# Kernel optimization log

Measured on AMD Instinct MI355X. Metric: run time of the kernel, lower is better.

Reference implementation:

```python
import jax, jax.numpy as jnp
import numpy as np
from jax import lax

BS, T, NN, F_IN = 4, 32, 128, 64
HID, HEADS, NC, LD, RH = 64, 4, 32, 64, 256
E = 2048
NEG_SLOPE = 0.2


def setup_inputs() -> dict:
    key = jax.random.key(0)
    ks = jax.random.split(key, 20)
    f32 = jnp.float32
    def n(k, shape, s=0.05):
        return jax.random.normal(k, shape, f32) * s
    G4 = 4 * RH
    return {
        "x": jax.random.normal(ks[0], (BS, T, NN, F_IN), f32),
        "edge_index": jax.random.randint(ks[1], (2, E), 0, NN),
        "W1": n(ks[2], (F_IN, HEADS * HID)),
        "as1": n(ks[3], (HEADS, HID)), "ad1": n(ks[4], (HEADS, HID)),
        "b1": jnp.zeros((HEADS * HID,), f32),
        "W2": n(ks[5], (HEADS * HID, HEADS * HID)),
        "as2": n(ks[6], (HEADS, HID)), "ad2": n(ks[7], (HEADS, HID)),
        "b2": jnp.zeros((HEADS * HID,), f32),
        "W3": n(ks[8], (HEADS * HID, HID)),
        "as3": n(ks[9], (1, HID)), "ad3": n(ks[10], (1, HID)),
        "b3": jnp.zeros((HID,), f32),
        "Wih_f": n(ks[11], (G4, HID)), "Whh_f": n(ks[12], (G4, RH)),
        "bih_f": jnp.zeros((G4,), f32), "bhh_f": jnp.zeros((G4,), f32),
        "Wih_b": n(ks[13], (G4, HID)), "Whh_b": n(ks[14], (G4, RH)),
        "bih_b": jnp.zeros((G4,), f32), "bhh_b": jnp.zeros((G4,), f32),
        "Wmu": n(ks[15], (NC * LD, 2 * RH)), "bmu": jnp.zeros((NC * LD,), f32),
        "Wlv": n(ks[16], (NC * LD, 2 * RH)), "blv": jnp.zeros((NC * LD,), f32),
        "Wpi": n(ks[17], (NC, 2 * RH)), "bpi": jnp.zeros((NC,), f32),
    }


def _lstm_dir(seq, Wih, Whh, bih, bhh, rh):
    # seq: [T, B, D]; torch gate order i, f, g, o
    B = seq.shape[1]
    h0 = jnp.zeros((B, rh), seq.dtype)
    c0 = jnp.zeros((B, rh), seq.dtype)
    def step(carry, xt):
        h, c = carry
        g = xt @ Wih.T + h @ Whh.T + bih + bhh
        i, f, gg, o = jnp.split(g, 4, axis=-1)
        c = jax.nn.sigmoid(f) * c + jax.nn.sigmoid(i) * jnp.tanh(gg)
        h = jax.nn.sigmoid(o) * jnp.tanh(c)
        return (h, c), None
    (hT, _), _ = lax.scan(step, (h0, c0), seq)
    return hT


def reference(x, edge_index, W1, as1, ad1, b1, W2, as2, ad2, b2,
              W3, as3, ad3, b3,
              Wih_f, Whh_f, bih_f, bhh_f, Wih_b, Whh_b, bih_b, bhh_b,
              Wmu, bmu, Wlv, blv, Wpi, bpi):
    bs, T_, nn_, fin = x.shape
    G = bs * T_
    N = G * nn_
    xt = x.reshape(N, fin)
    # batch the per-graph edge list with node offsets, then add self loops (PyG default)
    off = jnp.arange(G, dtype=edge_index.dtype) * nn_
    src = (edge_index[0][None, :] + off[:, None]).reshape(-1)
    dst = (edge_index[1][None, :] + off[:, None]).reshape(-1)
    loop = jnp.arange(N, dtype=edge_index.dtype)
    src = jnp.concatenate([src, loop])
    dst = jnp.concatenate([dst, loop])

    def gat(h_in, W, a_s, a_d, b, heads):
        C = W.shape[1] // heads
        h = (h_in @ W).reshape(N, heads, C)
        a_src = jnp.sum(h * a_s, axis=-1)  # [N, H]
        a_dst = jnp.sum(h * a_d, axis=-1)
        e = jax.nn.leaky_relu(a_src[src] + a_dst[dst], NEG_SLOPE)  # [Etot, H]
        m = jax.ops.segment_max(e, dst, num_segments=N)
        m = jnp.where(jnp.isfinite(m), m, 0.0)
        ex = jnp.exp(e - m[dst])
        den = jax.ops.segment_sum(ex, dst, num_segments=N)
        alpha = ex / (den[dst] + 1e-16)
        out = jax.ops.segment_sum(alpha[:, :, None] * h[src], dst, num_segments=N)
        return out.reshape(N, heads * C) + b

    h = jax.nn.relu(gat(xt, W1, as1, ad1, b1, HEADS))
    h = jax.nn.relu(gat(h, W2, as2, ad2, b2, HEADS))
    h = jax.nn.relu(gat(h, W3, as3, ad3, b3, 1))

    batch_idx = jnp.repeat(jnp.arange(G), nn_)
    graph_embs = jax.ops.segment_sum(h, batch_idx, num_segments=G).reshape(bs, T_, -1)
    seq = jnp.transpose(graph_embs, (1, 0, 2))  # [T, B, D]
    h_f = _lstm_dir(seq, Wih_f, Whh_f, bih_f, bhh_f, RH)
    h_b = _lstm_dir(seq[::-1], Wih_b, Whh_b, bih_b, bhh_b, RH)
    feat = jnp.concatenate([h_f, h_b], axis=-1)  # [B, 2*RH]
    mu = (feat @ Wmu.T + bmu).reshape(bs, NC, LD)
    logvar = (feat @ Wlv.T + blv).reshape(bs, NC, LD)
    pi_logits = feat @ Wpi.T + bpi
    return (mu, logvar, pi_logits)
```

## Files before the change

### kernel.cpp

```cpp
#include <hip/hip_runtime.h>
#include <hip/hip_bf16.h>
#include <cstdint>

#define NLOC 128
#define NGRAPH 128
#define NNODE 16384
#define EBASE 2048

typedef _Float16 half2v __attribute__((ext_vector_type(2)));
typedef _Float16 f16x8 __attribute__((ext_vector_type(8)));
typedef float f32x4 __attribute__((ext_vector_type(4)));

__device__ __forceinline__ float sigf(float x) { return 1.f / (1.f + __expf(-x)); }
__device__ __forceinline__ float tanhfast(float x) {
    float e = __expf(2.f * x);
    return 1.f - 2.f / (e + 1.f);
}
__device__ __forceinline__ uint32_t packh2(float a, float b) {
    half2v v;
    v.x = (_Float16)a; v.y = (_Float16)b;
    return __builtin_bit_cast(uint32_t, v);
}
__device__ __forceinline__ float dot2(uint32_t w, uint32_t h, float acc) {
#if __has_builtin(__builtin_amdgcn_fdot2)
    return __builtin_amdgcn_fdot2(__builtin_bit_cast(half2v, w),
                                  __builtin_bit_cast(half2v, h), acc, false);
#else
    half2v wv = __builtin_bit_cast(half2v, w);
    half2v hv = __builtin_bit_cast(half2v, h);
    return acc + (float)wv.x * (float)hv.x + (float)wv.y * (float)hv.y;
#endif
}

__global__ __launch_bounds__(256) void prep_kernel(const int* __restrict__ ei,
                                                   float* __restrict__ Adj,
                                                   const float* __restrict__ Whh_f,
                                                   const float* __restrict__ Whh_b,
                                                   uint32_t* __restrict__ wreg,
                                                   uint32_t* __restrict__ wtail) {
    int b = blockIdx.x, tid = threadIdx.x;
    if (b < 128) {
        __shared__ int rowA[NLOC];
        int v = b;
        if (tid < NLOC) rowA[tid] = 0;
        __syncthreads();
        const int* srcs = ei;
        const int* dsts = ei + EBASE;
        int e0 = tid * 8;
#pragma unroll
        for (int k = 0; k < 8; ++k)
            if (dsts[e0 + k] == v) atomicAdd(&rowA[srcs[e0 + k]], 1);
        __syncthreads();
        if (tid < NLOC) Adj[v * NLOC + tid] = (float)rowA[tid] + (tid == v ? 1.f : 0.f);
    } else {
        int gid = (b - 128) * 256 + tid;
        int dir = gid >> 10, row = gid & 1023;
        const float* src = (dir ? Whh_b : Whh_f) + (size_t)row * 256;
        uint4* wr4 = (uint4*)wreg;
#pragma unroll
        for (int i = 0; i < 24; ++i) {
            uint4 v;
            v.x = packh2(src[i * 8 + 0], src[i * 8 + 1]);
            v.y = packh2(src[i * 8 + 2], src[i * 8 + 3]);
            v.z = packh2(src[i * 8 + 4], src[i * 8 + 5]);
            v.w = packh2(src[i * 8 + 6], src[i * 8 + 7]);
            wr4[(size_t)(dir * 24 + i) * 1024 + row] = v;
        }
        uint4* wt4 = (uint4*)wtail;
#pragma unroll
        for (int ku = 0; ku < 8; ++ku) {
            const float* s8 = src + 192 + ku * 8;
            uint4 v;
            v.x = packh2(s8[0], s8[1]);
            v.y = packh2(s8[2], s8[3]);
            v.z = packh2(s8[4], s8[5]);
            v.w = packh2(s8[6], s8[7]);
            wt4[(size_t)(dir * 8 + ku) * 1024 + row] = v;
        }
    }
}

template <int K, int NL, int NF, bool POOLX>
__global__ __launch_bounds__(512) void fl_kernel(const float* __restrict__ A,
                                                 const float* __restrict__ Wg,
                                                 const float* __restrict__ a_s,
                                                 const float* __restrict__ a_d,
                                                 const float* __restrict__ Adj,
                                                 const float* __restrict__ bias,
                                                 const float* __restrict__ Wih_f, const float* __restrict__ bif, const float* __restrict__ bhf,
                                                 const float* __restrict__ Wih_b, const float* __restrict__ bib, const float* __restrict__ bhb,
                                                 float* __restrict__ outG) {
    constexpr int HL = NL / 64;
    constexpr int NT = NL / 64;
    constexpr int WPH = 4 / HL;
    constexpr int NLSH = (NL == 128) ? 7 : 6;
    constexpr int LDA = K + 4;
    constexpr int LDB = 68;
    constexpr int LDH = 136;
    constexpr int ASB = 128 * LDA * 2;
    constexpr int HTB = NL * LDH * 2;
    constexpr int R1 = (ASB > HTB) ? ASB : HTB;
    constexpr int R2 = 128 * LDH * 2;
    __shared__ __align__(16) char raw[R1 + R2];
    _Float16* As = (_Float16*)raw;
    _Float16* Ht = (_Float16*)raw;
    _Float16* Bs = (_Float16*)(raw + R1);
    _Float16* Wt = (_Float16*)(raw + R1);
    __shared__ float as_l[128 * HL];
    __shared__ float ad_l[128 * HL];
    __shared__ float den_l[128];
    __shared__ float as_part[4][128];
    __shared__ float ad_part[4][128];
    __shared__ float psum[8][64];
    __shared__ float emb[64];

    int g = blockIdx.x, tid = threadIdx.x;
    int foff = blockIdx.y * NL;
    int lane = tid & 63, w = tid >> 6;
    int wm = w >> 2, wn = w & 3;
    int col = lane & 15, kg = lane >> 4;
    size_t base = (size_t)g * 128;

    float asc[NT], adc[NT];
#pragma unroll
    for (int nt = 0; nt < NT; ++nt) {
        int f = foff + (wn * NT + nt) * 16 + col;
        asc[nt] = a_s[f];
        adc[nt] = a_d[f];
    }
    {
        const float* src = A + base * K;
        for (int i = tid; i < 128 * K / 2; i += 512) {
            int m = (2 * i) / K, k = (2 * i) % K;
            float2 v = *(const float2*)(src + (size_t)m * K + k);
            *(uint32_t*)&As[m * LDA + k] = packh2(v.x, v.y);
        }
    }
    f32x4 acc[4][NT];
#pragma unroll
    for (int mt = 0; mt < 4; ++mt)
#pragma unroll
        for (int nt = 0; nt < NT; ++nt) acc[mt][nt] = (f32x4){0.f, 0.f, 0.f, 0.f};
#pragma unroll 1
    for (int kc = 0; kc < K / 64; ++kc) {
        __syncthreads();
        for (int j = tid; j < NL * 32; j += 512) {
            int n = j & (NL - 1), kk = j >> NLSH;
            int k = kc * 64 + 2 * kk;
            float w0 = Wg[(size_t)k * NF + foff + n];
            float w1 = Wg[(size_t)(k + 1) * NF + foff + n];
            *(uint32_t*)&Bs[n * LDB + 2 * kk] = packh2(w0, w1);
        }
        __syncthreads();
        uint4 bf[NT][2];
#pragma unroll
        for (int nt = 0; nt < NT; ++nt) {
            int nb = (wn * NT + nt) * 16 + col;
            bf[nt][0] = *(const uint4*)&Bs[nb * LDB + kg * 8];
            bf[nt][1] = *(const uint4*)&Bs[nb * LDB + 32 + kg * 8];
        }
#pragma unroll
        for (int mt = 0; mt < 4; ++mt) {
            int mrow = wm * 64 + mt * 16 + col;
            uint4 a0 = *(const uint4*)&As[mrow * LDA + kc * 64 + kg * 8];
            uint4 a1 = *(const uint4*)&As[mrow * LDA + kc * 64 + 32 + kg * 8];
#pragma unroll
            for (int nt = 0; nt < NT; ++nt) {
                acc[mt][nt] = __builtin_amdgcn_mfma_f32_16x16x32_f16(
                    __builtin_bit_cast(f16x8, a0), __builtin_bit_cast(f16x8, bf[nt][0]),
                    acc[mt][nt], 0, 0, 0);
                acc[mt][nt] = __builtin_amdgcn_mfma_f32_16x16x32_f16(
                    __builtin_bit_cast(f16x8, a1), __builtin_bit_cast(f16x8, bf[nt][1]),
                    acc[mt][nt], 0, 0, 0);
            }
        }
    }
    __syncthreads();
#pragma unroll
    for (int mt = 0; mt < 4; ++mt) {
        int mb = wm * 64 + mt * 16;
        float pas[4] = {0.f, 0.f, 0.f, 0.f}, pdd[4] = {0.f, 0.f, 0.f, 0.f};
#pragma unroll
        for (int nt = 0; nt < NT; ++nt) {
#pragma unroll
            for (int r = 0; r < 4; ++r) {
                float hv = acc[mt][nt][r];
                pas[r] += hv * asc[nt];
                pdd[r] += hv * adc[nt];
            }
            int f = (wn * NT + nt) * 16 + col;
            *(uint32_t*)&Ht[f * LDH + mb + kg * 4] = packh2(acc[mt][nt][0], acc[mt][nt][1]);
            *(uint32_t*)&Ht[f * LDH + mb + kg * 4 + 2] = packh2(acc[mt][nt][2], acc[mt][nt][3]);
        }
#pragma unroll
        for (int off = 1; off < 16; off <<= 1)
#pragma unroll
            for (int r = 0; r < 4; ++r) {
                pas[r] += __shfl_xor(pas[r], off, 64);
                pdd[r] += __shfl_xor(pdd[r], off, 64);
            }
        if (col == 0) {
#pragma unroll
            for (int r = 0; r < 4; ++r) {
                int m = mb + kg * 4 + r;
                as_part[wn][m] = pas[r];
                ad_part[wn][m] = pdd[r];
            }
        }
    }
    __syncthreads();
    if (tid < 128) {
#pragma unroll
        for (int hl = 0; hl < HL; ++hl) {
            float sa = 0.f, sd = 0.f;
#pragma unroll
            for (int q = 0; q < WPH; ++q) {
                sa += as_part[hl * WPH + q][tid];
                sd += ad_part[hl * WPH + q][tid];
            }
            as_l[tid * HL + hl] = sa;
            ad_l[tid * HL + hl] = sd;
        }
    }
    __syncthreads();
    for (int h = 0; h < HL; ++h) {
        {
            int v = tid >> 2, ub = (tid & 3) * 32;
            float advv = ad_l[v * HL + h];
            const float* arow = Adj + (size_t)v * 128 + ub;
            float dsum = 0.f;
#pragma unroll
            for (int j = 0; j < 16; ++j) {
                float a0 = arow[2 * j], a1 = arow[2 * j + 1];
                float e0 = as_l[(ub + 2 * j) * HL + h] + advv;
                float e1 = as_l[(ub + 2 * j + 1) * HL + h] + advv;
                e0 = (e0 > 0.f) ? e0 : 0.2f * e0;
                e1 = (e1 > 0.f) ? e1 : 0.2f * e1;
                float w0 = a0 * __expf(e0);
                float w1 = a1 * __expf(e1);
                dsum += w0 + w1;
                *(uint32_t*)&Wt[v * LDH + ub + 2 * j] = packh2(w0, w1);
            }
            dsum += __shfl_xor(dsum, 1, 64);
            dsum += __shfl_xor(dsum, 2, 64);
            if ((tid & 3) == 0) den_l[v] = dsum;
        }
        __syncthreads();
        {
            int vt = w;
            f16x8 af[4];
#pragma unroll
            for (int kt = 0; kt < 4; ++kt) {
                uint4 au = *(const uint4*)&Wt[(vt * 16 + col) * LDH + kt * 32 + kg * 8];
                af[kt] = __builtin_bit_cast(f16x8, au);
            }
            float dn[4];
#pragma unroll
            for (int r = 0; r < 4; ++r) dn[r] = den_l[vt * 16 + kg * 4 + r] + 1e-16f;
#pragma unroll
            for (int ft = 0; ft < 4; ++ft) {
                int f = h * 64 + ft * 16 + col;
                f32x4 oacc = {0.f, 0.f, 0.f, 0.f};
#pragma unroll
                for (int kt = 0; kt < 4; ++kt) {
                    uint4 bu = *(const uint4*)&Ht[f * LDH + kt * 32 + kg * 8];
                    oacc = __builtin_amdgcn_mfma_f32_16x16x32_f16(
                        af[kt], __builtin_bit_cast(f16x8, bu), oacc, 0, 0, 0);
                }
                float bv = bias[foff + f];
                if constexpr (!POOLX) {
#pragma unroll
                    for (int r = 0; r < 4; ++r) {
                        int v = vt * 16 + kg * 4 + r;
                        float o = oacc[r] / dn[r] + bv;
                        outG[(size_t)(base + v) * NF + foff + f] = fmaxf(o, 0.f);
                    }
                } else {
                    float ps = 0.f;
#pragma unroll
                    for (int r = 0; r < 4; ++r) ps += fmaxf(oacc[r] / dn[r] + bv, 0.f);
                    ps += __shfl_xor(ps, 16, 64);
                    ps += __shfl_xor(ps, 32, 64);
                    if (kg == 0) psum[w][f] = ps;
                }
            }
        }
        __syncthreads();
    }
    if constexpr (POOLX) {
        if (tid < 64) {
            float s = 0.f;
#pragma unroll
            for (int q = 0; q < 8; ++q) s += psum[q][tid];
            emb[tid] = s;
        }
        __syncthreads();
        int rrow = (g & 31) * 4 + (g >> 5);
        for (int dir = 0; dir < 2; ++dir) {
            const float* W = dir ? Wih_b : Wih_f;
            const float* bi = dir ? bib : bif;
            const float* bh = dir ? bhb : bhf;
            for (int o = tid; o < 1024; o += 512) {
                const float* wr = W + (size_t)o * 64;
                float s = bi[o] + bh[o];
#pragma unroll
                for (int k = 0; k < 64; k += 4) {
                    float4 wv = *(const float4*)(wr + k);
                    s += emb[k] * wv.x + emb[k + 1] * wv.y + emb[k + 2] * wv.z + emb[k + 3] * wv.w;
                }
                outG[dir * 131072 + rrow * 1024 + o] = s;
            }
        }
    }
}

__global__ __launch_bounds__(1024, 1) void lstm_kernel(const float* __restrict__ xp,
                                                       const uint32_t* __restrict__ wreg,
                                                       const uint32_t* __restrict__ wtail,
                                                       float* __restrict__ hT) {
    int blk = blockIdx.x;
    int dir = blk >> 2, batch = blk & 3;
    int t = threadIdx.x;
    uint32_t wa[96];
    {
        const uint4* ra = (const uint4*)wreg + (size_t)dir * 24 * 1024;
#pragma unroll
        for (int i = 0; i < 24; ++i) {
            uint4 v = ra[i * 1024 + t];
            wa[i * 4 + 0] = v.x; wa[i * 4 + 1] = v.y; wa[i * 4 + 2] = v.z; wa[i * 4 + 3] = v.w;
        }
    }
    __shared__ __align__(16) uint4 wlds[8 * 1024];
    __shared__ __align__(16) uint32_t h_pk[128];
    __shared__ float gv[1024];
    {
        const uint4* tsrc = (const uint4*)wtail + (size_t)dir * 8 * 1024;
        for (int i = t; i < 8 * 1024; i += 1024) wlds[i] = tsrc[i];
    }
    if (t < 128) h_pk[t] = 0;
    __syncthreads();
    float creg = 0.f;
    const float* xpb = xp + dir * 131072 + batch * 1024;
#pragma unroll 1
    for (int step = 0; step < 32; ++step) {
        int teff = dir ? (31 - step) : step;
        float xa = xpb[teff * 4096 + t];
        float acc = 0.f;
#pragma unroll
        for (int q = 0; q < 24; ++q) {
            uint4 hq = *(const uint4*)&h_pk[q * 4];
            acc = dot2(wa[q * 4 + 0], hq.x, acc);
            acc = dot2(wa[q * 4 + 1], hq.y, acc);
            acc = dot2(wa[q * 4 + 2], hq.z, acc);
            acc = dot2(wa[q * 4 + 3], hq.w, acc);
        }
#pragma unroll
        for (int ku = 0; ku < 8; ++ku) {
            uint4 hq = *(const uint4*)&h_pk[96 + ku * 4];
            uint4 qa = wlds[ku * 1024 + t];
            acc = dot2(qa.x, hq.x, acc); acc = dot2(qa.y, hq.y, acc);
            acc = dot2(qa.z, hq.z, acc); acc = dot2(qa.w, hq.w, acc);
        }
        gv[t] = acc + xa;
        __syncthreads();
        if (t < 256) {
            float iv = gv[t], fv = gv[t + 256], gg = gv[t + 512], ov = gv[t + 768];
            creg = sigf(fv) * creg + sigf(iv) * tanhfast(gg);
            float hv = sigf(ov) * tanhfast(creg);
            if (step == 31) hT[(size_t)(dir * 4 + batch) * 256 + t] = hv;
            float hnext = __shfl_down(hv, 1, 64);
            if ((t & 1) == 0) h_pk[t >> 1] = packh2(hv, hnext);
        }
        __syncthreads();
    }
}

__global__ __launch_bounds__(256) void heads_kernel(const float* __restrict__ hT,
                                                    const float* __restrict__ Wmu, const float* __restrict__ bmu,
                                                    const float* __restrict__ Wlv, const float* __restrict__ blv,
                                                    const float* __restrict__ Wpi, const float* __restrict__ bpi,
                                                    float* __restrict__ out) {
    __shared__ __align__(16) float feat[4][512];
    int tid = threadIdx.x;
    for (int i = tid; i < 2048; i += 256) {
        int b = i >> 9, j = i & 511;
        int d = j >> 8, jj = j & 255;
        feat[b][j] = hT[(size_t)(d * 4 + b) * 256 + jj];
    }
    __syncthreads();
    int o = blockIdx.x * 32 + (tid >> 3);
    int kp = tid & 7;
    if (o >= 4128) return;
    const float* Wr;
    float bv;
    int kind, m;
    if (o < 2048) { Wr = Wmu + (size_t)o * 512; bv = bmu[o]; kind = 0; m = o; }
    else if (o < 4096) { m = o - 2048; Wr = Wlv + (size_t)m * 512; bv = blv[m]; kind = 1; }
    else { m = o - 4096; Wr = Wpi + (size_t)m * 512; bv = bpi[m]; kind = 2; }
    float s0 = 0.f, s1 = 0.f, s2 = 0.f, s3 = 0.f;
    int k0 = kp * 64;
#pragma unroll
    for (int j = 0; j < 16; ++j) {
        int k = k0 + j * 4;
        float4 wv = *(const float4*)(Wr + k);
        s0 += feat[0][k] * wv.x + feat[0][k + 1] * wv.y + feat[0][k + 2] * wv.z + feat[0][k + 3] * wv.w;
        s1 += feat[1][k] * wv.x + feat[1][k + 1] * wv.y + feat[1][k + 2] * wv.z + feat[1][k + 3] * wv.w;
        s2 += feat[2][k] * wv.x + feat[2][k + 1] * wv.y + feat[2][k + 2] * wv.z + feat[2][k + 3] * wv.w;
        s3 += feat[3][k] * wv.x + feat[3][k + 1] * wv.y + feat[3][k + 2] * wv.z + feat[3][k + 3] * wv.w;
    }
#pragma unroll
    for (int off = 1; off < 8; off <<= 1) {
        s0 += __shfl_xor(s0, off, 64);
        s1 += __shfl_xor(s1, off, 64);
        s2 += __shfl_xor(s2, off, 64);
        s3 += __shfl_xor(s3, off, 64);
    }
    if (kp != 0) return;
    s0 += bv; s1 += bv; s2 += bv; s3 += bv;
    if (kind == 0) {
        out[0 * 2048 + m] = s0; out[1 * 2048 + m] = s1; out[2 * 2048 + m] = s2; out[3 * 2048 + m] = s3;
    } else if (kind == 1) {
        out[8192 + 0 * 2048 + m] = s0; out[8192 + 1 * 2048 + m] = s1;
        out[8192 + 2 * 2048 + m] = s2; out[8192 + 3 * 2048 + m] = s3;
    } else {
        out[16384 + 0 * 32 + m] = s0; out[16384 + 1 * 32 + m] = s1;
        out[16384 + 2 * 32 + m] = s2; out[16384 + 3 * 32 + m] = s3;
    }
}

extern "C" void kernel_launch(void* const* d_in, const int* in_sizes, int n_in,
                              void* d_out, int out_size, void* d_ws, size_t ws_size,
                              hipStream_t stream) {
    const float* x = (const float*)d_in[0];
    const int* ei = (const int*)d_in[1];
    const float* W1 = (const float*)d_in[2];
    const float* as1 = (const float*)d_in[3];
    const float* ad1 = (const float*)d_in[4];
    const float* b1 = (const float*)d_in[5];
    const float* W2 = (const float*)d_in[6];
    const float* as2 = (const float*)d_in[7];
    const float* ad2 = (const float*)d_in[8];
    const float* b2 = (const float*)d_in[9];
    const float* W3 = (const float*)d_in[10];
    const float* as3 = (const float*)d_in[11];
    const float* ad3 = (const float*)d_in[12];
    const float* b3 = (const float*)d_in[13];
    const float* Wih_f = (const float*)d_in[14];
    const float* Whh_f = (const float*)d_in[15];
    const float* bih_f = (const float*)d_in[16];
    const float* bhh_f = (const float*)d_in[17];
    const float* Wih_b = (const float*)d_in[18];
    const float* Whh_b = (const float*)d_in[19];
    const float* bih_b = (const float*)d_in[20];
    const float* bhh_b = (const float*)d_in[21];
    const float* Wmu = (const float*)d_in[22];
    const float* bmu = (const float*)d_in[23];
    const float* Wlv = (const float*)d_in[24];
    const float* blv = (const float*)d_in[25];
    const float* Wpi = (const float*)d_in[26];
    const float* bpi = (const float*)d_in[27];

    float* ws = (float*)d_ws;
    float* buf1 = ws;
    float* buf2 = ws + 4194304;
    float* Adj = ws + 8388608;
    float* xp = ws + 8404992;
    float* hT = ws + 8667136;
    uint32_t* wreg = (uint32_t*)(ws + 8669184);
    uint32_t* wtail = wreg + 196608;
    float* out = (float*)d_out;

    prep_kernel<<<136, 256, 0, stream>>>(ei, Adj, Whh_f, Whh_b, wreg, wtail);
    fl_kernel<64, 128, 256, false><<<dim3(128, 2), 512, 0, stream>>>(x, W1, as1, ad1, Adj, b1,
        Wih_f, bih_f, bhh_f, Wih_b, bih_b, bhh_b, buf1);
    fl_kernel<256, 128, 256, false><<<dim3(128, 2), 512, 0, stream>>>(buf1, W2, as2, ad2, Adj, b2,
        Wih_f, bih_f, bhh_f, Wih_b, bih_b, bhh_b, buf2);
    fl_kernel<256, 64, 64, true><<<dim3(128, 1), 512, 0, stream>>>(buf2, W3, as3, ad3, Adj, b3,
        Wih_f, bih_f, bhh_f, Wih_b, bih_b, bhh_b, xp);
    lstm_kernel<<<8, 1024, 0, stream>>>(xp, wreg, wtail, hT);
    heads_kernel<<<129, 256, 0, stream>>>(hT, Wmu, bmu, Wlv, blv, Wpi, bpi, out);
}
```

Before: 196.2 us.

## Fuse three GAT layer kernels into one persistent kernel with per-graph flags

Result: slower. 261.1 us (+33.0%).

```diff
diff --git a/kernel.cpp b/kernel.cpp
--- a/kernel.cpp
+++ b/kernel.cpp
@@ -37,11 +37,14 @@
                                                    const float* __restrict__ Whh_f,
                                                    const float* __restrict__ Whh_b,
                                                    uint32_t* __restrict__ wreg,
-                                                   uint32_t* __restrict__ wtail) {
+                                                   uint32_t* __restrict__ wtail,
+                                                   int* __restrict__ gflag1,
+                                                   int* __restrict__ gflag2) {
     int b = blockIdx.x, tid = threadIdx.x;
     if (b < 128) {
         __shared__ int rowA[NLOC];
         int v = b;
+        if (tid == 0) { gflag1[v] = 0; gflag2[v] = 0; }
         if (tid < NLOC) rowA[tid] = 0;
         __syncthreads();
         const int* srcs = ei;
@@ -81,15 +84,19 @@
 }
 
 template <int K, int NL, int NF, bool POOLX>
-__global__ __launch_bounds__(512) void fl_kernel(const float* __restrict__ A,
-                                                 const float* __restrict__ Wg,
-                                                 const float* __restrict__ a_s,
-                                                 const float* __restrict__ a_d,
-                                                 const float* __restrict__ Adj,
-                                                 const float* __restrict__ bias,
-                                                 const float* __restrict__ Wih_f, const float* __restrict__ bif, const float* __restrict__ bhf,
-                                                 const float* __restrict__ Wih_b, const float* __restrict__ bib, const float* __restrict__ bhb,
-                                                 float* __restrict__ outG) {
+__device__ void fl_body(int g, int foff,
+                        const float* __restrict__ A,
+                        const float* __restrict__ Wg,
+                        const float* __restrict__ a_s,
+                        const float* __restrict__ a_d,
+                        const float* __restrict__ Adj,
+                        const float* __restrict__ bias,
+                        const float* __restrict__ Wih_f, const float* __restrict__ bif, const float* __restrict__ bhf,
+                        const float* __restrict__ Wih_b, const float* __restrict__ bib, const float* __restrict__ bhb,
+                        float* __restrict__ outG,
+                        char* raw, float* as_l, float* ad_l, float* den_l,
+                        float (*as_part)[128], float (*ad_part)[128],
+                        float (*psum)[64], float* emb) {
     constexpr int HL = NL / 64;
     constexpr int NT = NL / 64;
     constexpr int WPH = 4 / HL;
@@ -100,22 +107,12 @@
     constexpr int ASB = 128 * LDA * 2;
     constexpr int HTB = NL * LDH * 2;
     constexpr int R1 = (ASB > HTB) ? ASB : HTB;
-    constexpr int R2 = 128 * LDH * 2;
-    __shared__ __align__(16) char raw[R1 + R2];
     _Float16* As = (_Float16*)raw;
     _Float16* Ht = (_Float16*)raw;
     _Float16* Bs = (_Float16*)(raw + R1);
     _Float16* Wt = (_Float16*)(raw + R1);
-    __shared__ float as_l[128 * HL];
-    __shared__ float ad_l[128 * HL];
-    __shared__ float den_l[128];
-    __shared__ float as_part[4][128];
-    __shared__ float ad_part[4][128];
-    __shared__ float psum[8][64];
-    __shared__ float emb[64];
-
-    int g = blockIdx.x, tid = threadIdx.x;
-    int foff = blockIdx.y * NL;
+
+    int tid = threadIdx.x;
     int lane = tid & 63, w = tid >> 6;
     int wm = w >> 2, wn = w & 3;
     int col = lane & 15, kg = lane >> 4;
@@ -312,6 +309,54 @@
             }
         }
     }
+}
+
+struct MegaArgs {
+    const float* x;
+    const float* W1; const float* as1; const float* ad1; const float* b1;
+    const float* W2; const float* as2; const float* ad2; const float* b2;
+    const float* W3; const float* as3; const float* ad3; const float* b3;
+    const float* Wih_f; const float* bif; const float* bhf;
+    const float* Wih_b; const float* bib; const float* bhb;
+    const float* Adj;
+    float* buf1; float* buf2; float* xp;
+    int* gflag1; int* gflag2;
+};
+
+__global__ __launch_bounds__(512) void gat_mega(MegaArgs a) {
+    __shared__ __align__(16) char raw[101376];
+    __shared__ float as_l[256], ad_l[256], den_l[128];
+    __shared__ float as_part[4][128], ad_part[4][128];
+    __shared__ float psum[8][64], emb[64];
+    int b = blockIdx.x, tid = threadIdx.x;
+    int g = b & 127, hb = b >> 7;
+    fl_body<64, 128, 256, false>(g, hb * 128, a.x, a.W1, a.as1, a.ad1, a.Adj, a.b1,
+        a.Wih_f, a.bif, a.bhf, a.Wih_b, a.bib, a.bhb, a.buf1,
+        raw, as_l, ad_l, den_l, as_part, ad_part, psum, emb);
+    __threadfence();
+    __syncthreads();
+    if (tid == 0) {
+        atomicAdd(&a.gflag1[g], 1);
+        while (__hip_atomic_load(&a.gflag1[g], __ATOMIC_ACQUIRE, __HIP_MEMORY_SCOPE_AGENT) < 2)
+            __builtin_amdgcn_s_sleep(1);
+    }
+    __syncthreads();
+    fl_body<256, 128, 256, false>(g, hb * 128, a.buf1, a.W2, a.as2, a.ad2, a.Adj, a.b2,
+        a.Wih_f, a.bif, a.bhf, a.Wih_b, a.bib, a.bhb, a.buf2,
+        raw, as_l, ad_l, den_l, as_part, ad_part, psum, emb);
+    __threadfence();
+    __syncthreads();
+    if (tid == 0) {
+        atomicAdd(&a.gflag2[g], 1);
+        if (hb == 0)
+            while (__hip_atomic_load(&a.gflag2[g], __ATOMIC_ACQUIRE, __HIP_MEMORY_SCOPE_AGENT) < 2)
+                __builtin_amdgcn_s_sleep(1);
+    }
+    if (hb != 0) return;
+    __syncthreads();
+    fl_body<256, 64, 64, true>(g, 0, a.buf2, a.W3, a.as3, a.ad3, a.Adj, a.b3,
+        a.Wih_f, a.bif, a.bhf, a.Wih_b, a.bib, a.bhb, a.xp,
+        raw, as_l, ad_l, den_l, as_part, ad_part, psum, emb);
 }
 
 __global__ __launch_bounds__(1024, 1) void lstm_kernel(const float* __restrict__ xp,
@@ -468,15 +513,24 @@
     float* hT = ws + 8667136;
     uint32_t* wreg = (uint32_t*)(ws + 8669184);
     uint32_t* wtail = wreg + 196608;
+    int* gflag1 = (int*)(wtail + 65536);
+    int* gflag2 = gflag1 + 128;
     float* out = (float*)d_out;
 
-    prep_kernel<<<136, 256, 0, stream>>>(ei, Adj, Whh_f, Whh_b, wreg, wtail);
-    fl_kernel<64, 128, 256, false><<<dim3(128, 2), 512, 0, stream>>>(x, W1, as1, ad1, Adj, b1,
-        Wih_f, bih_f, bhh_f, Wih_b, bih_b, bhh_b, buf1);
-    fl_kernel<256, 128, 256, false><<<dim3(128, 2), 512, 0, stream>>>(buf1, W2, as2, ad2, Adj, b2,
-        Wih_f, bih_f, bhh_f, Wih_b, bih_b, bhh_b, buf2);
-    fl_kernel<256, 64, 64, true><<<dim3(128, 1), 512, 0, stream>>>(buf2, W3, as3, ad3, Adj, b3,
-        Wih_f, bih_f, bhh_f, Wih_b, bih_b, bhh_b, xp);
+    prep_kernel<<<136, 256, 0, stream>>>(ei, Adj, Whh_f, Whh_b, wreg, wtail, gflag1, gflag2);
+
+    MegaArgs ma;
+    ma.x = x;
+    ma.W1 = W1; ma.as1 = as1; ma.ad1 = ad1; ma.b1 = b1;
+    ma.W2 = W2; ma.as2 = as2; ma.ad2 = ad2; ma.b2 = b2;
+    ma.W3 = W3; ma.as3 = as3; ma.ad3 = ad3; ma.b3 = b3;
+    ma.Wih_f = Wih_f; ma.bif = bih_f; ma.bhf = bhh_f;
+    ma.Wih_b = Wih_b; ma.bib = bih_b; ma.bhb = bhh_b;
+    ma.Adj = Adj;
+    ma.buf1 = buf1; ma.buf2 = buf2; ma.xp = xp;
+    ma.gflag1 = gflag1; ma.gflag2 = gflag2;
+    gat_mega<<<256, 512, 0, stream>>>(ma);
+
     lstm_kernel<<<8, 1024, 0, stream>>>(xp, wreg, wtail, hT);
     heads_kernel<<<129, 256, 0, stream>>>(hT, Wmu, bmu, Wlv, blv, Wpi, bpi, out);
 }
```
